# Kernel optimization log

Measured on AMD Instinct MI355X. Metric: run time of the kernel, lower is better.

Reference implementation:

```python
import jax, jax.numpy as jnp
import numpy as np

NC = 50000
NG = 2000
D = 64
NE = 1000000
NP = 500000
BN_EPS = 1e-5


def setup_inputs() -> dict:
    key = jax.random.key(0)
    ks = jax.random.split(key, 16)
    return {
        "cell_feat1": jax.random.normal(ks[0], (NC, D), jnp.float32) * 0.05,
        "cell_feat2": jax.random.normal(ks[1], (NC, D), jnp.float32) * 0.05,
        "gene_feat": jax.random.normal(ks[2], (NG, D), jnp.float32) * 0.05,
        "emb_W": jax.random.normal(ks[3], (D + 2, D), jnp.float32) * 0.05,
        "emb_b": jnp.zeros((D,), jnp.float32),
        "bn_gamma": jnp.ones((D,), jnp.float32),
        "bn_beta": jnp.zeros((D,), jnp.float32),
        "bn_mean": jnp.zeros((D,), jnp.float32),
        "bn_var": jnp.ones((D,), jnp.float32),
        "enc_src1": jax.random.randint(ks[4], (NE,), 0, NC, jnp.int32),
        "enc_dst1": jax.random.randint(ks[5], (NE,), 0, NG, jnp.int32),
        "enc_src2": jax.random.randint(ks[6], (NE,), 0, NC, jnp.int32),
        "enc_dst2": jax.random.randint(ks[7], (NE,), 0, NG, jnp.int32),
        "pos_src1": jax.random.randint(ks[8], (NP,), 0, NC, jnp.int32),
        "pos_dst1": jax.random.randint(ks[9], (NP,), 0, NG, jnp.int32),
        "pos_src2": jax.random.randint(ks[10], (NP,), 0, NC, jnp.int32),
        "pos_dst2": jax.random.randint(ks[11], (NP,), 0, NG, jnp.int32),
    }


def _inv_sqrt_deg(idx, n):
    # deg^{-1/2} per node, 0 for isolated nodes; shape (n, 1)
    deg = jax.ops.segment_sum(jnp.ones_like(idx, jnp.float32), idx, num_segments=n)
    return jnp.where(deg > 0, jax.lax.rsqrt(jnp.maximum(deg, 1.0)), 0.0)[:, None]


def reference(cell_feat1, cell_feat2, gene_feat, emb_W, emb_b,
              bn_gamma, bn_beta, bn_mean, bn_var,
              enc_src1, enc_dst1, enc_src2, enc_dst2,
              pos_src1, pos_dst1, pos_src2, pos_dst2):
    nc, ng = cell_feat1.shape[0], gene_feat.shape[0]
    # degree normalizers per relation (cj = src deg^-1/2, ci = dst deg^-1/2)
    cj_c1 = _inv_sqrt_deg(enc_src1, nc)
    ci_g1 = _inv_sqrt_deg(enc_dst1, ng)
    cj_c2 = _inv_sqrt_deg(enc_src2, nc)
    ci_g2 = _inv_sqrt_deg(enc_dst2, ng)

    def spmm(src_feats, cj, src_idx, dst_idx, ci, n_dst):
        # gather-scale-scatter-scale: ci * sum_{j in N(i)} cj_j * h_j
        msgs = (src_feats * cj)[src_idx]
        return ci * jax.ops.segment_sum(msgs, dst_idx, num_segments=n_dst)

    def layer(c1, c2, g):
        # cell -> gene (two edge types, HeteroGraphConv aggregate='mean')
        g1 = spmm(c1, cj_c1, enc_src1, enc_dst1, ci_g1, ng)
        g2 = spmm(c2, cj_c2, enc_src2, enc_dst2, ci_g2, ng)
        g_new = 0.5 * (g1 + g2)
        # gene -> cell (reverse edges; roles of ci/cj swap)
        c1_new = spmm(g, ci_g1, enc_dst1, enc_src1, cj_c1, nc)
        c2_new = spmm(g, ci_g2, enc_dst2, enc_src2, cj_c2, nc)
        return c1_new, c2_new, g_new

    w = jnp.float32(1.0 / 3.0)  # n_layers == 2 -> weights [1/3, 1/3, 1/3]
    u1, u2, ih = w * cell_feat1, w * cell_feat2, w * gene_feat
    c1, c2, g = cell_feat1, cell_feat2, gene_feat
    for _ in range(2):
        c1, c2, g = layer(c1, c2, g)
        u1 = u1 + w * c1
        u2 = u2 + w * c2
        ih = ih + w * g

    # emb_layer: Linear(d+2 -> d) on [feat | batch one-hot], BN (eval), ELU
    def emb(u, onehot):
        x = jnp.concatenate([u, jnp.broadcast_to(onehot, (u.shape[0], 2))], axis=1)
        y = x @ emb_W + emb_b
        y = bn_gamma * (y - bn_mean) * jax.lax.rsqrt(bn_var + BN_EPS) + bn_beta
        return jax.nn.elu(y)

    uf1 = emb(u1, jnp.array([1.0, 0.0], jnp.float32))
    uf2 = emb(u2, jnp.array([0.0, 1.0], jnp.float32))

    # DotDecoder: per-positive-edge dot product
    pred1 = jnp.sum(uf1[pos_src1] * ih[pos_dst1], axis=1)
    pred2 = jnp.sum(uf2[pos_src2] * ih[pos_dst2], axis=1)
    return jnp.concatenate([pred1, pred2])
```

## Files before the change

### kernel.cpp

```cpp
#include <hip/hip_runtime.h>
#include <math.h>

#define NC   50000
#define NG   2000
#define DD   64
#define NE   1000000
#define NPOS 500000
#define WTH  (1.0f/3.0f)

#define GSTRIDE 640
#define CSTRIDE 64

#define NRNGB  256
#define RNGCB  196
#define RCAP   4608
#define NRNGG  250
#define GPRG   8
#define RCAPG  4608
#define CHUNKB 4096

typedef unsigned short u16;
typedef unsigned char  u8;

__device__ __forceinline__ float bf2f(u16 u) {
    return __uint_as_float(((unsigned)u) << 16);
}
__device__ __forceinline__ u16 f2bf(float f) {
    unsigned x = __float_as_uint(f);
    return (u16)((x + 0x7FFFu + ((x >> 16) & 1u)) >> 16);
}
__device__ __forceinline__ float blo(unsigned u) { return __uint_as_float(u << 16); }
__device__ __forceinline__ float bhi(unsigned u) { return __uint_as_float(u & 0xFFFF0000u); }

__global__ __launch_bounds__(256) void k_bin2(
    const int* __restrict__ s1, const int* __restrict__ d1,
    const int* __restrict__ s2, const int* __restrict__ d2,
    int* __restrict__ rcnt_c1, int* __restrict__ rcnt_c2,
    int* __restrict__ rcnt_g1, int* __restrict__ rcnt_g2,
    unsigned* __restrict__ rbc1, unsigned* __restrict__ rbc2,
    unsigned* __restrict__ rbg1, unsigned* __restrict__ rbg2)
{
    __shared__ unsigned ed[CHUNKB];
    __shared__ unsigned hc[NRNGB], bc[NRNGB];
    __shared__ unsigned hg[NRNGG], bg[NRNGG];
    const int* src; const int* dst; int* rc; int* rg; unsigned* rbc; unsigned* rbg;
    if (blockIdx.y == 0) { src = s1; dst = d1; rc = rcnt_c1; rg = rcnt_g1; rbc = rbc1; rbg = rbg1; }
    else                 { src = s2; dst = d2; rc = rcnt_c2; rg = rcnt_g2; rbc = rbc2; rbg = rbg2; }
    int t = threadIdx.x;
    if (t < NRNGB) hc[t] = 0;
    if (t < NRNGG) hg[t] = 0;
    __syncthreads();
    int e0 = blockIdx.x * CHUNKB;
    #pragma unroll 4
    for (int i = 0; i < CHUNKB / 256; i++) {
        int e = e0 + i * 256 + t;
        unsigned pk = 0xFFFFFFFFu;
        if (e < NE) {
            int s = src[e], g = dst[e];
            pk = ((unsigned)s << 16) | (unsigned)g;
            atomicAdd(&hc[s / RNGCB], 1u);
            atomicAdd(&hg[g >> 3], 1u);
        }
        ed[i * 256 + t] = pk;
    }
    __syncthreads();
    if (t < NRNGB) { unsigned c = hc[t]; bc[t] = c ? (unsigned)atomicAdd(&rc[t], (int)c) : 0u; hc[t] = 0; }
    if (t < NRNGG) { unsigned c = hg[t]; bg[t] = c ? (unsigned)atomicAdd(&rg[t], (int)c) : 0u; hg[t] = 0; }
    __syncthreads();
    #pragma unroll 4
    for (int i = 0; i < CHUNKB / 256; i++) {
        unsigned pk = ed[i * 256 + t];
        if (pk != 0xFFFFFFFFu) {
            int s = (int)(pk >> 16), g = (int)(pk & 0xFFFFu);
            int r1 = s / RNGCB;
            unsigned p = bc[r1] + atomicAdd(&hc[r1], 1u);
            if (p < RCAP)
                rbc[(size_t)r1 * RCAP + p] = ((unsigned)(s - r1 * RNGCB) << 16) | (unsigned)g;
            int r2 = g >> 3;
            unsigned q = bg[r2] + atomicAdd(&hg[r2], 1u);
            if (q < RCAPG)
                rbg[(size_t)r2 * RCAPG + q] = ((unsigned)(g & 7) << 16) | (unsigned)s;
        }
    }
}

__global__ __launch_bounds__(256) void k_binfill(
    const int* __restrict__ rcnt1, const int* __restrict__ rcnt2,
    const unsigned* __restrict__ rbuf1, const unsigned* __restrict__ rbuf2,
    u16* __restrict__ adj_c1, u16* __restrict__ adj_c2,
    int* __restrict__ cnt_c1, int* __restrict__ cnt_c2)
{
    __shared__ u16 rows[RNGCB * CSTRIDE];
    __shared__ unsigned cur[(RNGCB + 3) / 4];
    const int* rcnt; const unsigned* rbuf; u16* adj; int* cnt;
    if (blockIdx.y == 0) { rcnt = rcnt1; rbuf = rbuf1; adj = adj_c1; cnt = cnt_c1; }
    else                 { rcnt = rcnt2; rbuf = rbuf2; adj = adj_c2; cnt = cnt_c2; }
    int t = threadIdx.x;
    int r = blockIdx.x;
    if (t < (RNGCB + 3) / 4) cur[t] = 0;
    __syncthreads();
    int n = rcnt[r]; if (n > RCAP) n = RCAP;
    const unsigned* buf = rbuf + (size_t)r * RCAP;
    for (int i = t; i < n; i += 256) {
        unsigned e = buf[i];
        unsigned cl = e >> 16;
        unsigned sh = 8u * (cl & 3u);
        unsigned old = atomicAdd(&cur[cl >> 2], 1u << sh);
        unsigned p = (old >> sh) & 0xFFu;
        if (p < CSTRIDE) rows[cl * CSTRIDE + p] = (u16)(e & 0xFFFFu);
    }
    __syncthreads();
    int lo = r * RNGCB;
    int valid = NC - lo; if (valid > RNGCB) valid = RNGCB;
    if (valid <= 0) return;
    if (t < valid) {
        unsigned p = (cur[t >> 2] >> (8u * (t & 3u))) & 0xFFu;
        cnt[lo + t] = (int)((p > CSTRIDE) ? CSTRIDE : p);
    }
    uint4* gd = (uint4*)(adj + (size_t)lo * CSTRIDE);
    const uint4* ls = (const uint4*)rows;
    for (int i = t; i < valid * (CSTRIDE / 8); i += 256) gd[i] = ls[i];
}

__global__ __launch_bounds__(256) void k_binfill_g(
    const int* __restrict__ rcnt1, const int* __restrict__ rcnt2,
    const unsigned* __restrict__ rbuf1, const unsigned* __restrict__ rbuf2,
    u16* __restrict__ adj_g1, u16* __restrict__ adj_g2,
    int* __restrict__ cnt_g1, int* __restrict__ cnt_g2)
{
    __shared__ u16 rows[GPRG * GSTRIDE];
    __shared__ unsigned cur[GPRG];
    const int* rcnt; const unsigned* rbuf; u16* adj; int* cnt;
    if (blockIdx.y == 0) { rcnt = rcnt1; rbuf = rbuf1; adj = adj_g1; cnt = cnt_g1; }
    else                 { rcnt = rcnt2; rbuf = rbuf2; adj = adj_g2; cnt = cnt_g2; }
    int t = threadIdx.x;
    int r = blockIdx.x;
    if (t < GPRG) cur[t] = 0;
    __syncthreads();
    int n = rcnt[r]; if (n > RCAPG) n = RCAPG;
    const unsigned* buf = rbuf + (size_t)r * RCAPG;
    for (int i = t; i < n; i += 256) {
        unsigned e = buf[i];
        unsigned gl = e >> 16;
        unsigned p = atomicAdd(&cur[gl], 1u);
        if (p < GSTRIDE) rows[gl * GSTRIDE + p] = (u16)(e & 0xFFFFu);
    }
    __syncthreads();
    if (t < GPRG) {
        unsigned p = cur[t];
        cnt[r * GPRG + t] = (int)((p > GSTRIDE) ? GSTRIDE : p);
    }
    uint4* gd = (uint4*)(adj + (size_t)r * GPRG * GSTRIDE);
    const uint4* ls = (const uint4*)rows;
    for (int i = t; i < GPRG * GSTRIDE / 8; i += 256) gd[i] = ls[i];
}

__global__ __launch_bounds__(256) void k_prep(
    const int* __restrict__ cnt_c1, const int* __restrict__ cnt_c2,
    const int* __restrict__ cnt_g1, const int* __restrict__ cnt_g2,
    const float* __restrict__ cell1, const float* __restrict__ cell2,
    const float* __restrict__ gfeat,
    float* __restrict__ cj_c1, float* __restrict__ cj_c2,
    float* __restrict__ ci_g1, float* __restrict__ ci_g2,
    u16* __restrict__ t1s, u16* __restrict__ t2s,
    u16* __restrict__ gf1s, u16* __restrict__ gf2s)
{
    int i = blockIdx.x * 4 + (threadIdx.x >> 6);
    int d = threadIdx.x & 63;
    if (i < NC) {
        int a = cnt_c1[i]; float j1 = (a > 0) ? 1.0f / sqrtf((float)a) : 0.0f;
        int b = cnt_c2[i]; float j2 = (b > 0) ? 1.0f / sqrtf((float)b) : 0.0f;
        if (d == 0) { cj_c1[i] = j1; cj_c2[i] = j2; }
        int idx = i * DD + d;
        t1s[idx] = f2bf(cell1[idx] * j1);
        t2s[idx] = f2bf(cell2[idx] * j2);
    }
    if (i < NG) {
        int a = cnt_g1[i]; float j1 = (a > 0) ? 1.0f / sqrtf((float)a) : 0.0f;
        int b = cnt_g2[i]; float j2 = (b > 0) ? 1.0f / sqrtf((float)b) : 0.0f;
        if (d == 0) { ci_g1[i] = j1; ci_g2[i] = j2; }
        int idx = i * DD + d;
        float g = gfeat[idx];
        gf1s[idx] = f2bf(g * j1);
        gf2s[idx] = f2bf(g * j2);
    }
}

__global__ __launch_bounds__(256) void k_c2g(
    const u16* __restrict__ src1s, const u16* __restrict__ src2s,
    const u16* __restrict__ adj_g1, const int* __restrict__ cnt_g1,
    const u16* __restrict__ adj_g2, const int* __restrict__ cnt_g2,
    const float* __restrict__ ci_g1, const float* __restrict__ ci_g2,
    u16* __restrict__ gb1s, u16* __restrict__ gb2s,
    const float* __restrict__ gfeat_init,
    float* __restrict__ ih, u16* __restrict__ ihb)
{
    __shared__ float l1[4][DD];
    __shared__ float l2[4][DD];
    int i   = blockIdx.x;
    int d   = threadIdx.x & 63;
    int grp = threadIdx.x >> 6;

    int n1 = cnt_g1[i]; if (n1 > GSTRIDE) n1 = GSTRIDE;
    const u16* a1 = adj_g1 + i * GSTRIDE;
    float acc1 = 0.f;
    int e = grp;
    for (; e + 28 < n1; e += 32) {
        int s0 = a1[e],      s1 = a1[e + 4],  s2 = a1[e + 8],  s3 = a1[e + 12];
        int s4 = a1[e + 16], s5 = a1[e + 20], s6 = a1[e + 24], s7 = a1[e + 28];
        float v0 = bf2f(src1s[s0 * DD + d]), v1 = bf2f(src1s[s1 * DD + d]);
        float v2 = bf2f(src1s[s2 * DD + d]), v3 = bf2f(src1s[s3 * DD + d]);
        float v4 = bf2f(src1s[s4 * DD + d]), v5 = bf2f(src1s[s5 * DD + d]);
        float v6 = bf2f(src1s[s6 * DD + d]), v7 = bf2f(src1s[s7 * DD + d]);
        acc1 += ((v0 + v1) + (v2 + v3)) + ((v4 + v5) + (v6 + v7));
    }
    for (; e < n1; e += 4) acc1 += bf2f(src1s[a1[e] * DD + d]);

    int n2 = cnt_g2[i]; if (n2 > GSTRIDE) n2 = GSTRIDE;
    const u16* a2 = adj_g2 + i * GSTRIDE;
    float acc2 = 0.f;
    e = grp;
    for (; e + 28 < n2; e += 32) {
        int s0 = a2[e],      s1 = a2[e + 4],  s2 = a2[e + 8],  s3 = a2[e + 12];
        int s4 = a2[e + 16], s5 = a2[e + 20], s6 = a2[e + 24], s7 = a2[e + 28];
        float v0 = bf2f(src2s[s0 * DD + d]), v1 = bf2f(src2s[s1 * DD + d]);
        float v2 = bf2f(src2s[s2 * DD + d]), v3 = bf2f(src2s[s3 * DD + d]);
        float v4 = bf2f(src2s[s4 * DD + d]), v5 = bf2f(src2s[s5 * DD + d]);
        float v6 = bf2f(src2s[s6 * DD + d]), v7 = bf2f(src2s[s7 * DD + d]);
        acc2 += ((v0 + v1) + (v2 + v3)) + ((v4 + v5) + (v6 + v7));
    }
    for (; e < n2; e += 4) acc2 += bf2f(src2s[a2[e] * DD + d]);

    l1[grp][d] = acc1; l2[grp][d] = acc2;
    __syncthreads();
    if (grp == 0) {
        float s1 = l1[0][d] + l1[1][d] + l1[2][d] + l1[3][d];
        float s2 = l2[0][d] + l2[1][d] + l2[2][d] + l2[3][d];
        float ci1 = ci_g1[i], ci2 = ci_g2[i];
        float gn = 0.5f * (ci1 * s1 + ci2 * s2);
        int idx = i * DD + d;
        if (gb1s) { gb1s[idx] = f2bf(gn * ci1); gb2s[idx] = f2bf(gn * ci2); }
        if (gfeat_init) ih[idx] = WTH * (gfeat_init[idx] + gn);
        else            ihb[idx] = f2bf(ih[idx] + WTH * gn);
    }
}

__global__ __launch_bounds__(256) void k_g2c(
    const u16* __restrict__ g1s, const u16* __restrict__ g2s,
    const u16* __restrict__ adj_c1, const int* __restrict__ cnt_c1,
    const u16* __restrict__ adj_c2, const int* __restrict__ cnt_c2,
    const float* __restrict__ cj_c1, const float* __restrict__ cj_c2,
    const float* __restrict__ cf1_init, const float* __restrict__ cf2_init,
    u16* __restrict__ c1bs, u16* __restrict__ c2bs,
    float* __restrict__ u1, float* __restrict__ u2)
{
    int i = blockIdx.x * 4 + (threadIdx.x >> 6);
    if (i >= NC) return;
    int d = threadIdx.x & 63;

    int n1 = cnt_c1[i]; if (n1 > CSTRIDE) n1 = CSTRIDE;
    int n2 = cnt_c2[i]; if (n2 > CSTRIDE) n2 = CSTRIDE;
    const u16* a1 = adj_c1 + (size_t)i * CSTRIDE;
    const u16* a2 = adj_c2 + (size_t)i * CSTRIDE;
    float acc1 = 0.f, acc2 = 0.f;
    int e1 = 0, e2 = 0;
    int m1 = n1 & ~3, m2 = n2 & ~3;
    int m = (m1 < m2) ? m1 : m2;
    for (; e1 < m; e1 += 4, e2 += 4) {
        int j0 = a1[e1], j1 = a1[e1 + 1], j2 = a1[e1 + 2], j3 = a1[e1 + 3];
        int k0 = a2[e2], k1 = a2[e2 + 1], k2 = a2[e2 + 2], k3 = a2[e2 + 3];
        float p0 = bf2f(g1s[j0 * DD + d]), p1 = bf2f(g1s[j1 * DD + d]);
        float p2 = bf2f(g1s[j2 * DD + d]), p3 = bf2f(g1s[j3 * DD + d]);
        float q0 = bf2f(g2s[k0 * DD + d]), q1 = bf2f(g2s[k1 * DD + d]);
        float q2 = bf2f(g2s[k2 * DD + d]), q3 = bf2f(g2s[k3 * DD + d]);
        acc1 += (p0 + p1) + (p2 + p3);
        acc2 += (q0 + q1) + (q2 + q3);
    }
    for (; e1 + 3 < n1; e1 += 4) {
        int j0 = a1[e1], j1 = a1[e1 + 1], j2 = a1[e1 + 2], j3 = a1[e1 + 3];
        acc1 += (bf2f(g1s[j0 * DD + d]) + bf2f(g1s[j1 * DD + d]))
              + (bf2f(g1s[j2 * DD + d]) + bf2f(g1s[j3 * DD + d]));
    }
    for (; e1 < n1; e1++) acc1 += bf2f(g1s[a1[e1] * DD + d]);
    for (; e2 + 3 < n2; e2 += 4) {
        int k0 = a2[e2], k1 = a2[e2 + 1], k2 = a2[e2 + 2], k3 = a2[e2 + 3];
        acc2 += (bf2f(g2s[k0 * DD + d]) + bf2f(g2s[k1 * DD + d]))
              + (bf2f(g2s[k2 * DD + d]) + bf2f(g2s[k3 * DD + d]));
    }
    for (; e2 < n2; e2++) acc2 += bf2f(g2s[a2[e2] * DD + d]);

    float jc1 = cj_c1[i];
    float jc2 = cj_c2[i];
    float c1n = jc1 * acc1;
    float c2n = jc2 * acc2;

    int idx = i * DD + d;
    if (cf1_init) {
        u1[idx] = WTH * (cf1_init[idx] + c1n);
        u2[idx] = WTH * (cf2_init[idx] + c2n);
        c1bs[idx] = f2bf(c1n * jc1);
        c2bs[idx] = f2bf(c2n * jc2);
    } else {
        u1[idx] += WTH * c1n;
        u2[idx] += WTH * c2n;
    }
}

__global__ __launch_bounds__(256, 4) void k_emb(
    const float* __restrict__ u1, const float* __restrict__ u2,
    u16* __restrict__ uf1b, u16* __restrict__ uf2b,
    const float* __restrict__ W, const float* __restrict__ bb,
    const float* __restrict__ gam, const float* __restrict__ bet,
    const float* __restrict__ mea, const float* __restrict__ var)
{
    int d = threadIdx.x & 63;
    int wid = blockIdx.x * 4 + (threadIdx.x >> 6);
    int nw = gridDim.x * 4;

    float Wl[DD];
    #pragma unroll
    for (int k = 0; k < DD; k++) Wl[k] = W[k * DD + d];
    float inv = 1.0f / sqrtf(var[d] + 1e-5f);
    float ga = gam[d], be = bet[d], me = mea[d];
    float bias1 = bb[d] + W[DD * DD + d];
    float bias2 = bb[d] + W[(DD + 1) * DD + d];

    for (int r = wid; r < 2 * NC; r += nw) {
        int which = (r >= NC) ? 1 : 0;
        int row = which ? (r - NC) : r;
        const float* u = which ? u2 : u1;
        float xv = u[(size_t)row * DD + d];
        float y = which ? bias2 : bias1;
        #pragma unroll
        for (int k = 0; k < DD; k++) {
            float xk = __uint_as_float(
                (unsigned)__builtin_amdgcn_readlane(__float_as_uint(xv), k));
            y += xk * Wl[k];
        }
        float t = ga * (y - me) * inv + be;
        t = (t > 0.f) ? t : expm1f(t);
        u16* ob = which ? uf2b : uf1b;
        ob[(size_t)row * DD + d] = f2bf(t);
    }
}

__global__ __launch_bounds__(256) void k_dec(
    const u16* __restrict__ uf1b, const u16* __restrict__ uf2b,
    const u16* __restrict__ ihb,
    const int* __restrict__ ps1, const int* __restrict__ pd1,
    const int* __restrict__ ps2, const int* __restrict__ pd2,
    float* __restrict__ out)
{
    int t = blockIdx.x * 256 + threadIdx.x;
    int e = t >> 3;
    int l = t & 7;
    if (e >= 2 * NPOS) return;
    const u16* uf; int s, g;
    if (e < NPOS) { uf = uf1b; s = ps1[e];        g = pd1[e];        }
    else          { uf = uf2b; s = ps2[e - NPOS]; g = pd2[e - NPOS]; }
    uint4 av = ((const uint4*)(uf + (size_t)s * DD))[l];
    uint4 cv = ((const uint4*)(ihb + (size_t)g * DD))[l];
    float acc = blo(av.x) * blo(cv.x) + bhi(av.x) * bhi(cv.x)
              + blo(av.y) * blo(cv.y) + bhi(av.y) * bhi(cv.y)
              + blo(av.z) * blo(cv.z) + bhi(av.z) * bhi(cv.z)
              + blo(av.w) * blo(cv.w) + bhi(av.w) * bhi(cv.w);
    acc += __shfl_xor(acc, 4);
    acc += __shfl_xor(acc, 2);
    acc += __shfl_xor(acc, 1);
    if (l == 0) out[e] = acc;
}

extern "C" void kernel_launch(void* const* d_in, const int* in_sizes, int n_in,
                              void* d_out, int out_size, void* d_ws, size_t ws_size,
                              hipStream_t stream)
{
    const float* cell1 = (const float*)d_in[0];
    const float* cell2 = (const float*)d_in[1];
    const float* gfeat = (const float*)d_in[2];
    const float* embW  = (const float*)d_in[3];
    const float* embB  = (const float*)d_in[4];
    const float* bng   = (const float*)d_in[5];
    const float* bnb   = (const float*)d_in[6];
    const float* bnm   = (const float*)d_in[7];
    const float* bnv   = (const float*)d_in[8];
    const int* es1 = (const int*)d_in[9];
    const int* ed1 = (const int*)d_in[10];
    const int* es2 = (const int*)d_in[11];
    const int* ed2 = (const int*)d_in[12];
    const int* ps1 = (const int*)d_in[13];
    const int* pd1 = (const int*)d_in[14];
    const int* ps2 = (const int*)d_in[15];
    const int* pd2 = (const int*)d_in[16];
    float* out = (float*)d_out;

    char* base = (char*)d_ws;
    size_t off = 0;
    auto alloc = [&](size_t bytes) -> void* {
        void* p = base + off;
        off = (off + bytes + 255) & ~(size_t)255;
        return p;
    };
    int* rcnt_c1 = (int*)alloc((size_t)NRNGB * 4);
    int* rcnt_c2 = (int*)alloc((size_t)NRNGB * 4);
    int* rcnt_g1 = (int*)alloc((size_t)NRNGG * 4);
    int* rcnt_g2 = (int*)alloc((size_t)NRNGG * 4);
    size_t cntEnd = off;
    int* cnt_c1 = (int*)alloc((size_t)NC * 4);
    int* cnt_c2 = (int*)alloc((size_t)NC * 4);
    int* cnt_g1 = (int*)alloc((size_t)NG * 4);
    int* cnt_g2 = (int*)alloc((size_t)NG * 4);
    float* u1 = (float*)alloc((size_t)NC * DD * 4);
    float* u2 = (float*)alloc((size_t)NC * DD * 4);
    unsigned* rbc1 = (unsigned*)u1;
    unsigned* rbc2 = rbc1 + (size_t)NRNGB * RCAP;
    unsigned* rbg1 = (unsigned*)u2;
    unsigned* rbg2 = rbg1 + (size_t)NRNGG * RCAPG;
    u16* adj_c1 = (u16*)alloc((size_t)NC * CSTRIDE * 2);
    u16* adj_c2 = (u16*)alloc((size_t)NC * CSTRIDE * 2);
    u16* adj_g1 = (u16*)alloc((size_t)NG * GSTRIDE * 2);
    u16* adj_g2 = (u16*)alloc((size_t)NG * GSTRIDE * 2);
    float* cj_c1 = (float*)alloc((size_t)NC * 4);
    float* cj_c2 = (float*)alloc((size_t)NC * 4);
    float* ci_g1 = (float*)alloc((size_t)NG * 4);
    float* ci_g2 = (float*)alloc((size_t)NG * 4);
    u16* t1s  = (u16*)alloc((size_t)NC * DD * 2);
    u16* t2s  = (u16*)alloc((size_t)NC * DD * 2);
    u16* c1bs = (u16*)alloc((size_t)NC * DD * 2);
    u16* c2bs = (u16*)alloc((size_t)NC * DD * 2);
    u16* gf1s = (u16*)alloc((size_t)NG * DD * 2);
    u16* gf2s = (u16*)alloc((size_t)NG * DD * 2);
    u16* gb1s = (u16*)alloc((size_t)NG * DD * 2);
    u16* gb2s = (u16*)alloc((size_t)NG * DD * 2);
    float* ih  = (float*)alloc((size_t)NG * DD * 4);
    u16*   ihb = (u16*)alloc((size_t)NG * DD * 2);
    (void)ws_size; (void)in_sizes; (void)n_in; (void)out_size;

    hipMemsetAsync(d_ws, 0, cntEnd, stream);

    dim3 gr((NE + CHUNKB - 1) / CHUNKB, 2);
    k_bin2<<<gr, 256, 0, stream>>>(es1, ed1, es2, ed2,
                                   rcnt_c1, rcnt_c2, rcnt_g1, rcnt_g2,
                                   rbc1, rbc2, rbg1, rbg2);
    dim3 gf(NRNGB, 2);
    k_binfill<<<gf, 256, 0, stream>>>(rcnt_c1, rcnt_c2, rbc1, rbc2,
                                      adj_c1, adj_c2, cnt_c1, cnt_c2);
    dim3 gg(NRNGG, 2);
    k_binfill_g<<<gg, 256, 0, stream>>>(rcnt_g1, rcnt_g2, rbg1, rbg2,
                                        adj_g1, adj_g2, cnt_g1, cnt_g2);
    k_prep<<<(NC + 3) / 4, 256, 0, stream>>>(cnt_c1, cnt_c2, cnt_g1, cnt_g2,
                                             cell1, cell2, gfeat,
                                             cj_c1, cj_c2, ci_g1, ci_g2,
                                             t1s, t2s, gf1s, gf2s);

    k_c2g<<<NG, 256, 0, stream>>>(t1s, t2s, adj_g1, cnt_g1, adj_g2, cnt_g2,
                                  ci_g1, ci_g2, gb1s, gb2s, gfeat, ih, nullptr);
    k_g2c<<<(NC + 3) / 4, 256, 0, stream>>>(gf1s, gf2s, adj_c1, cnt_c1, adj_c2, cnt_c2,
                                            cj_c1, cj_c2, cell1, cell2,
                                            c1bs, c2bs, u1, u2);
    k_c2g<<<NG, 256, 0, stream>>>(c1bs, c2bs, adj_g1, cnt_g1, adj_g2, cnt_g2,
                                  ci_g1, ci_g2, nullptr, nullptr, nullptr, ih, ihb);
    k_g2c<<<(NC + 3) / 4, 256, 0, stream>>>(gb1s, gb2s, adj_c1, cnt_c1, adj_c2, cnt_c2,
                                            cj_c1, cj_c2, nullptr, nullptr,
                                            nullptr, nullptr, u1, u2);
    k_emb<<<512, 256, 0, stream>>>(u1, u2, t1s, t2s,
                                   embW, embB, bng, bnb, bnm, bnv);
    k_dec<<<(2 * NPOS * 8 + 255) / 256, 256, 0, stream>>>(t1s, t2s, ihb,
                                                          ps1, pd1, ps2, pd2, out);
}
```

Baseline: 417.8 us.

## Fuse final cell aggregation into embedding kernel and vectorize adjacency index loads

```diff
diff --git a/kernel.cpp b/kernel.cpp
--- a/kernel.cpp
+++ b/kernel.cpp
@@ -204,32 +204,34 @@
     int n1 = cnt_g1[i]; if (n1 > GSTRIDE) n1 = GSTRIDE;
     const u16* a1 = adj_g1 + i * GSTRIDE;
     float acc1 = 0.f;
-    int e = grp;
-    for (; e + 28 < n1; e += 32) {
-        int s0 = a1[e],      s1 = a1[e + 4],  s2 = a1[e + 8],  s3 = a1[e + 12];
-        int s4 = a1[e + 16], s5 = a1[e + 20], s6 = a1[e + 24], s7 = a1[e + 28];
+    int e = 0;
+    for (; e + 32 <= n1; e += 32) {
+        uint4 w = *(const uint4*)(a1 + e + grp * 8);
+        int s0 = w.x & 0xFFFF, s1 = w.x >> 16, s2 = w.y & 0xFFFF, s3 = w.y >> 16;
+        int s4 = w.z & 0xFFFF, s5 = w.z >> 16, s6 = w.w & 0xFFFF, s7 = w.w >> 16;
         float v0 = bf2f(src1s[s0 * DD + d]), v1 = bf2f(src1s[s1 * DD + d]);
         float v2 = bf2f(src1s[s2 * DD + d]), v3 = bf2f(src1s[s3 * DD + d]);
         float v4 = bf2f(src1s[s4 * DD + d]), v5 = bf2f(src1s[s5 * DD + d]);
         float v6 = bf2f(src1s[s6 * DD + d]), v7 = bf2f(src1s[s7 * DD + d]);
         acc1 += ((v0 + v1) + (v2 + v3)) + ((v4 + v5) + (v6 + v7));
     }
-    for (; e < n1; e += 4) acc1 += bf2f(src1s[a1[e] * DD + d]);
+    for (int q = e + grp; q < n1; q += 4) acc1 += bf2f(src1s[a1[q] * DD + d]);
 
     int n2 = cnt_g2[i]; if (n2 > GSTRIDE) n2 = GSTRIDE;
     const u16* a2 = adj_g2 + i * GSTRIDE;
     float acc2 = 0.f;
-    e = grp;
-    for (; e + 28 < n2; e += 32) {
-        int s0 = a2[e],      s1 = a2[e + 4],  s2 = a2[e + 8],  s3 = a2[e + 12];
-        int s4 = a2[e + 16], s5 = a2[e + 20], s6 = a2[e + 24], s7 = a2[e + 28];
+    e = 0;
+    for (; e + 32 <= n2; e += 32) {
+        uint4 w = *(const uint4*)(a2 + e + grp * 8);
+        int s0 = w.x & 0xFFFF, s1 = w.x >> 16, s2 = w.y & 0xFFFF, s3 = w.y >> 16;
+        int s4 = w.z & 0xFFFF, s5 = w.z >> 16, s6 = w.w & 0xFFFF, s7 = w.w >> 16;
         float v0 = bf2f(src2s[s0 * DD + d]), v1 = bf2f(src2s[s1 * DD + d]);
         float v2 = bf2f(src2s[s2 * DD + d]), v3 = bf2f(src2s[s3 * DD + d]);
         float v4 = bf2f(src2s[s4 * DD + d]), v5 = bf2f(src2s[s5 * DD + d]);
         float v6 = bf2f(src2s[s6 * DD + d]), v7 = bf2f(src2s[s7 * DD + d]);
         acc2 += ((v0 + v1) + (v2 + v3)) + ((v4 + v5) + (v6 + v7));
     }
-    for (; e < n2; e += 4) acc2 += bf2f(src2s[a2[e] * DD + d]);
+    for (int q = e + grp; q < n2; q += 4) acc2 += bf2f(src2s[a2[q] * DD + d]);
 
     l1[grp][d] = acc1; l2[grp][d] = acc2;
     __syncthreads();
@@ -267,8 +269,10 @@
     int m1 = n1 & ~3, m2 = n2 & ~3;
     int m = (m1 < m2) ? m1 : m2;
     for (; e1 < m; e1 += 4, e2 += 4) {
-        int j0 = a1[e1], j1 = a1[e1 + 1], j2 = a1[e1 + 2], j3 = a1[e1 + 3];
-        int k0 = a2[e2], k1 = a2[e2 + 1], k2 = a2[e2 + 2], k3 = a2[e2 + 3];
+        uint2 w1 = *(const uint2*)(a1 + e1);
+        uint2 w2 = *(const uint2*)(a2 + e2);
+        int j0 = w1.x & 0xFFFF, j1 = w1.x >> 16, j2 = w1.y & 0xFFFF, j3 = w1.y >> 16;
+        int k0 = w2.x & 0xFFFF, k1 = w2.x >> 16, k2 = w2.y & 0xFFFF, k3 = w2.y >> 16;
         float p0 = bf2f(g1s[j0 * DD + d]), p1 = bf2f(g1s[j1 * DD + d]);
         float p2 = bf2f(g1s[j2 * DD + d]), p3 = bf2f(g1s[j3 * DD + d]);
         float q0 = bf2f(g2s[k0 * DD + d]), q1 = bf2f(g2s[k1 * DD + d]);
@@ -277,13 +281,15 @@
         acc2 += (q0 + q1) + (q2 + q3);
     }
     for (; e1 + 3 < n1; e1 += 4) {
-        int j0 = a1[e1], j1 = a1[e1 + 1], j2 = a1[e1 + 2], j3 = a1[e1 + 3];
+        uint2 w1 = *(const uint2*)(a1 + e1);
+        int j0 = w1.x & 0xFFFF, j1 = w1.x >> 16, j2 = w1.y & 0xFFFF, j3 = w1.y >> 16;
         acc1 += (bf2f(g1s[j0 * DD + d]) + bf2f(g1s[j1 * DD + d]))
               + (bf2f(g1s[j2 * DD + d]) + bf2f(g1s[j3 * DD + d]));
     }
     for (; e1 < n1; e1++) acc1 += bf2f(g1s[a1[e1] * DD + d]);
     for (; e2 + 3 < n2; e2 += 4) {
-        int k0 = a2[e2], k1 = a2[e2 + 1], k2 = a2[e2 + 2], k3 = a2[e2 + 3];
+        uint2 w2 = *(const uint2*)(a2 + e2);
+        int k0 = w2.x & 0xFFFF, k1 = w2.x >> 16, k2 = w2.y & 0xFFFF, k3 = w2.y >> 16;
         acc2 += (bf2f(g2s[k0 * DD + d]) + bf2f(g2s[k1 * DD + d]))
               + (bf2f(g2s[k2 * DD + d]) + bf2f(g2s[k3 * DD + d]));
     }
@@ -295,18 +301,17 @@
     float c2n = jc2 * acc2;
 
     int idx = i * DD + d;
-    if (cf1_init) {
-        u1[idx] = WTH * (cf1_init[idx] + c1n);
-        u2[idx] = WTH * (cf2_init[idx] + c2n);
-        c1bs[idx] = f2bf(c1n * jc1);
-        c2bs[idx] = f2bf(c2n * jc2);
-    } else {
-        u1[idx] += WTH * c1n;
-        u2[idx] += WTH * c2n;
-    }
-}
-
-__global__ __launch_bounds__(256, 4) void k_emb(
+    u1[idx] = WTH * (cf1_init[idx] + c1n);
+    u2[idx] = WTH * (cf2_init[idx] + c2n);
+    c1bs[idx] = f2bf(c1n * jc1);
+    c2bs[idx] = f2bf(c2n * jc2);
+}
+
+__global__ __launch_bounds__(256, 4) void k_g2c_emb(
+    const u16* __restrict__ g1s, const u16* __restrict__ g2s,
+    const u16* __restrict__ adj_c1, const int* __restrict__ cnt_c1,
+    const u16* __restrict__ adj_c2, const int* __restrict__ cnt_c2,
+    const float* __restrict__ cj_c1, const float* __restrict__ cj_c2,
     const float* __restrict__ u1, const float* __restrict__ u2,
     u16* __restrict__ uf1b, u16* __restrict__ uf2b,
     const float* __restrict__ W, const float* __restrict__ bb,
@@ -325,22 +330,61 @@
     float bias1 = bb[d] + W[DD * DD + d];
     float bias2 = bb[d] + W[(DD + 1) * DD + d];
 
-    for (int r = wid; r < 2 * NC; r += nw) {
-        int which = (r >= NC) ? 1 : 0;
-        int row = which ? (r - NC) : r;
-        const float* u = which ? u2 : u1;
-        float xv = u[(size_t)row * DD + d];
-        float y = which ? bias2 : bias1;
+    for (int i = wid; i < NC; i += nw) {
+        int n1 = cnt_c1[i]; if (n1 > CSTRIDE) n1 = CSTRIDE;
+        int n2 = cnt_c2[i]; if (n2 > CSTRIDE) n2 = CSTRIDE;
+        const u16* a1 = adj_c1 + (size_t)i * CSTRIDE;
+        const u16* a2 = adj_c2 + (size_t)i * CSTRIDE;
+        float acc1 = 0.f, acc2 = 0.f;
+        int e1 = 0, e2 = 0;
+        int m1 = n1 & ~3, m2 = n2 & ~3;
+        int m = (m1 < m2) ? m1 : m2;
+        for (; e1 < m; e1 += 4, e2 += 4) {
+            uint2 w1 = *(const uint2*)(a1 + e1);
+            uint2 w2 = *(const uint2*)(a2 + e2);
+            int j0 = w1.x & 0xFFFF, j1 = w1.x >> 16, j2 = w1.y & 0xFFFF, j3 = w1.y >> 16;
+            int k0 = w2.x & 0xFFFF, k1 = w2.x >> 16, k2 = w2.y & 0xFFFF, k3 = w2.y >> 16;
+            float p0 = bf2f(g1s[j0 * DD + d]), p1 = bf2f(g1s[j1 * DD + d]);
+            float p2 = bf2f(g1s[j2 * DD + d]), p3 = bf2f(g1s[j3 * DD + d]);
+            float q0 = bf2f(g2s[k0 * DD + d]), q1 = bf2f(g2s[k1 * DD + d]);
+            float q2 = bf2f(g2s[k2 * DD + d]), q3 = bf2f(g2s[k3 * DD + d]);
+            acc1 += (p0 + p1) + (p2 + p3);
+            acc2 += (q0 + q1) + (q2 + q3);
+        }
+        for (; e1 + 3 < n1; e1 += 4) {
+            uint2 w1 = *(const uint2*)(a1 + e1);
+            int j0 = w1.x & 0xFFFF, j1 = w1.x >> 16, j2 = w1.y & 0xFFFF, j3 = w1.y >> 16;
+            acc1 += (bf2f(g1s[j0 * DD + d]) + bf2f(g1s[j1 * DD + d]))
+                  + (bf2f(g1s[j2 * DD + d]) + bf2f(g1s[j3 * DD + d]));
+        }
+        for (; e1 < n1; e1++) acc1 += bf2f(g1s[a1[e1] * DD + d]);
+        for (; e2 + 3 < n2; e2 += 4) {
+            uint2 w2 = *(const uint2*)(a2 + e2);
+            int k0 = w2.x & 0xFFFF, k1 = w2.x >> 16, k2 = w2.y & 0xFFFF, k3 = w2.y >> 16;
+            acc2 += (bf2f(g2s[k0 * DD + d]) + bf2f(g2s[k1 * DD + d]))
+                  + (bf2f(g2s[k2 * DD + d]) + bf2f(g2s[k3 * DD + d]));
+        }
+        for (; e2 < n2; e2++) acc2 += bf2f(g2s[a2[e2] * DD + d]);
+
+        int idx = i * DD + d;
+        float x1 = u1[idx] + WTH * (cj_c1[i] * acc1);
+        float x2 = u2[idx] + WTH * (cj_c2[i] * acc2);
+        float y1 = bias1, y2 = bias2;
         #pragma unroll
         for (int k = 0; k < DD; k++) {
-            float xk = __uint_as_float(
-                (unsigned)__builtin_amdgcn_readlane(__float_as_uint(xv), k));
-            y += xk * Wl[k];
+            float xa = __uint_as_float(
+                (unsigned)__builtin_amdgcn_readlane(__float_as_uint(x1), k));
+            float xb = __uint_as_float(
+                (unsigned)__builtin_amdgcn_readlane(__float_as_uint(x2), k));
+            y1 += xa * Wl[k];
+            y2 += xb * Wl[k];
         }
-        float t = ga * (y - me) * inv + be;
-        t = (t > 0.f) ? t : expm1f(t);
-        u16* ob = which ? uf2b : uf1b;
-        ob[(size_t)row * DD + d] = f2bf(t);
+        float t1 = ga * (y1 - me) * inv + be;
+        t1 = (t1 > 0.f) ? t1 : expm1f(t1);
+        float t2 = ga * (y2 - me) * inv + be;
+        t2 = (t2 > 0.f) ? t2 : expm1f(t2);
+        uf1b[idx] = f2bf(t1);
+        uf2b[idx] = f2bf(t2);
     }
 }
 
@@ -459,11 +503,9 @@
                                             c1bs, c2bs, u1, u2);
     k_c2g<<<NG, 256, 0, stream>>>(c1bs, c2bs, adj_g1, cnt_g1, adj_g2, cnt_g2,
                                   ci_g1, ci_g2, nullptr, nullptr, nullptr, ih, ihb);
-    k_g2c<<<(NC + 3) / 4, 256, 0, stream>>>(gb1s, gb2s, adj_c1, cnt_c1, adj_c2, cnt_c2,
-                                            cj_c1, cj_c2, nullptr, nullptr,
-                                            nullptr, nullptr, u1, u2);
-    k_emb<<<512, 256, 0, stream>>>(u1, u2, t1s, t2s,
-                                   embW, embB, bng, bnb, bnm, bnv);
+    k_g2c_emb<<<2048, 256, 0, stream>>>(gb1s, gb2s, adj_c1, cnt_c1, adj_c2, cnt_c2,
+                                        cj_c1, cj_c2, u1, u2, t1s, t2s,
+                                        embW, embB, bng, bnb, bnm, bnv);
     k_dec<<<(2 * NPOS * 8 + 255) / 256, 256, 0, stream>>>(t1s, t2s, ihb,
                                                           ps1, pd1, ps2, pd2, out);
 }
```

Result: faster. 397.5 us (-4.9%).
